# Optimization experiments

Measured on AMD Instinct MI355X. Metric: run time of the kernel, lower is better.

## Reference

```python
import jax, jax.numpy as jnp
import numpy as np

B = 4096          # batch
N_REPS = 16       # number of irreducible reps (all same d here)
N_ELEMS = 128     # group elements per rep
D = 32            # block dimension
N_SYMBOLS = 64    # alphabet size
EMB = N_REPS * D * D  # 16384


def setup_inputs() -> dict:
    key = jax.random.key(0)
    k1, k2, k3, k4 = jax.random.split(key, 4)
    state_embedding = jax.random.normal(k1, (B, EMB), dtype=jnp.float32)
    input_symbols = jax.random.randint(k2, (B,), 0, N_SYMBOLS, dtype=jnp.int64)
    reps = jax.random.normal(k3, (N_REPS, N_ELEMS, D, D), dtype=jnp.float32)
    transitions = jax.random.randint(k4, (N_SYMBOLS,), 0, N_ELEMS, dtype=jnp.int64)
    return {"state_embedding": state_embedding, "input_symbols": input_symbols,
            "reps": reps, "transitions": transitions}


def reference(state_embedding, input_symbols, reps, transitions):
    # state_embedding: [B, n_reps*d*d]; reps: [n_reps, n_elems, d, d]
    n_reps, n_elems, d, _ = reps.shape
    b = state_embedding.shape[0]
    # Split embedding into block-diagonal d x d blocks (all reps same d).
    blocks = jnp.nan_to_num(state_embedding.reshape(b, n_reps, d, d))  # [b, r, d, d]
    # Per-symbol gather: symbol -> group element -> rep matrix.
    t = transitions[input_symbols]            # [b]
    M = jnp.nan_to_num(reps[:, t])            # [r, b, d, d]
    # Per-matrix Frobenius normalization (matches rep_matrix.norm()).
    fro = jnp.sqrt(jnp.sum(M * M, axis=(-2, -1), keepdims=True))
    M = M / (fro + 1e-6)
    # Block-diagonal batched matmul: block @ rep_matrix per (batch, rep).
    out = jnp.einsum('brij,rbjk->brik', blocks, M)  # [b, r, d, d]
    return out.reshape(b, -1)
```

## Files before the change

kernel.cpp:

```cpp
#include <hip/hip_runtime.h>
#include <hip/hip_bf16.h>

#define NREPS   16
#define NELEMS  128
#define DD      32
#define MATSZ   (DD * DD)
#define EMB     (NREPS * MATSZ)

typedef __attribute__((ext_vector_type(8))) short bf16x8;
typedef __attribute__((ext_vector_type(4))) float f32x4;

static __device__ __forceinline__ short f2bf(float f) {
    __hip_bfloat16 h = __float2bfloat16(f);
    return *reinterpret_cast<short*>(&h);
}

__global__ __launch_bounds__(256) void prep_kernel(
    const float* __restrict__ reps, ushort* __restrict__ Mt)
{
    __shared__ float lM[DD * 33];
    __shared__ float red[4];
    const int mat = blockIdx.x;
    const int t   = threadIdx.x;

    float4 v = reinterpret_cast<const float4*>(reps + (size_t)mat * MATSZ)[t];
    const int i  = t >> 3;
    const int c0 = (t & 7) << 2;
    lM[i * 33 + c0 + 0] = v.x;
    lM[i * 33 + c0 + 1] = v.y;
    lM[i * 33 + c0 + 2] = v.z;
    lM[i * 33 + c0 + 3] = v.w;

    float s = v.x * v.x + v.y * v.y + v.z * v.z + v.w * v.w;
    #pragma unroll
    for (int off = 32; off; off >>= 1) s += __shfl_xor(s, off, 64);
    if ((t & 63) == 0) red[t >> 6] = s;
    __syncthreads();
    const float scale = 1.0f / (sqrtf(red[0] + red[1] + red[2] + red[3]) + 1e-6f);

    const int col = t >> 3;
    const int k0  = (t & 7) << 2;
    ushort4 o;
    o.x = (ushort)f2bf(lM[(k0 + 0) * 33 + col] * scale);
    o.y = (ushort)f2bf(lM[(k0 + 1) * 33 + col] * scale);
    o.z = (ushort)f2bf(lM[(k0 + 2) * 33 + col] * scale);
    o.w = (ushort)f2bf(lM[(k0 + 3) * 33 + col] * scale);
    reinterpret_cast<ushort4*>(Mt + (size_t)mat * MATSZ)[t] = o;
}

__global__ __launch_bounds__(256, 4) void trans_mfma4_kernel(
    const float*  __restrict__ emb,
    const int*    __restrict__ syms,
    const ushort* __restrict__ Mt,
    const int*    __restrict__ trans,
    float*        __restrict__ out)
{
    const int b = blockIdx.x;
    const int w = threadIdx.x >> 6;
    const int l = threadIdx.x & 63;
    const int rr = w << 2;

    const int esym = trans[syms[b]];
    const int lr = l & 15;
    const int k0 = (l >> 4) << 3;

    const float*  A0 = emb + (size_t)b * EMB + (size_t)rr * MATSZ;
    const ushort* M0 = Mt + ((size_t)rr * NELEMS + esym) * MATSZ;

    float4 alo[4][2], ahi[4][2];
    bf16x8 bfg[4][2];
    #pragma unroll
    for (int p = 0; p < 4; ++p) {
        const float*  A = A0 + p * MATSZ;
        const ushort* M = M0 + (size_t)p * NELEMS * MATSZ;
        #pragma unroll
        for (int ti = 0; ti < 2; ++ti) {
            const float* ap = A + (ti * 16 + lr) * DD + k0;
            alo[p][ti] = *reinterpret_cast<const float4*>(ap);
            ahi[p][ti] = *reinterpret_cast<const float4*>(ap + 4);
        }
        #pragma unroll
        for (int tj = 0; tj < 2; ++tj)
            bfg[p][tj] = *reinterpret_cast<const bf16x8*>(M + (tj * 16 + lr) * DD + k0);
    }

    const f32x4 z = {0.0f, 0.0f, 0.0f, 0.0f};
    const int row0 = (l >> 4) << 2;

    #pragma unroll
    for (int p = 0; p < 4; ++p) {
        bf16x8 af[2];
        #pragma unroll
        for (int ti = 0; ti < 2; ++ti) {
            bf16x8 f;
            f[0] = f2bf(alo[p][ti].x); f[1] = f2bf(alo[p][ti].y);
            f[2] = f2bf(alo[p][ti].z); f[3] = f2bf(alo[p][ti].w);
            f[4] = f2bf(ahi[p][ti].x); f[5] = f2bf(ahi[p][ti].y);
            f[6] = f2bf(ahi[p][ti].z); f[7] = f2bf(ahi[p][ti].w);
            af[ti] = f;
        }

        f32x4 acc[2][2];
        #pragma unroll
        for (int ti = 0; ti < 2; ++ti)
            #pragma unroll
            for (int tj = 0; tj < 2; ++tj)
                acc[ti][tj] = __builtin_amdgcn_mfma_f32_16x16x32_bf16(
                    af[ti], bfg[p][tj], z, 0, 0, 0);

        float* Ob = out + (size_t)b * EMB + (size_t)(rr + p) * MATSZ;
        #pragma unroll
        for (int ti = 0; ti < 2; ++ti)
            #pragma unroll
            for (int m = 0; m < 4; ++m) {
                const int row = ti * 16 + row0 + m;
                #pragma unroll
                for (int tj = 0; tj < 2; ++tj)
                    __builtin_nontemporal_store(acc[ti][tj][m],
                                                Ob + row * DD + tj * 16 + lr);
            }
    }
}

extern "C" void kernel_launch(void* const* d_in, const int* in_sizes, int n_in,
                              void* d_out, int out_size, void* d_ws, size_t ws_size,
                              hipStream_t stream) {
    const float* emb   = (const float*)d_in[0];
    const int*   syms  = (const int*)d_in[1];
    const float* reps  = (const float*)d_in[2];
    const int*   trans = (const int*)d_in[3];
    float*  outp = (float*)d_out;
    ushort* Mt   = (ushort*)d_ws;

    const int B = in_sizes[1];

    hipLaunchKernelGGL(prep_kernel, dim3(NREPS * NELEMS), dim3(256), 0, stream,
                       reps, Mt);
    hipLaunchKernelGGL(trans_mfma4_kernel, dim3(B), dim3(256), 0, stream,
                       emb, syms, Mt, trans, outp);
}
```

Baseline: 119.9 us.

## Double-buffer per-matrix loads and process two batch rows per block

Replaces the load-everything-then-compute scheme with a two-slot register double buffer. Loads for the next matrix are issued while the current one is converted, multiplied and stored. Each block now covers two batch rows (8 matrices per wave), which halves the grid and lowers peak register use. The launch-bounds occupancy hint is dropped, so there are fewer loads in flight per wave, and the gain depends on the compiler keeping the loads ahead of the stores.

```diff
diff --git a/kernel.cpp b/kernel.cpp
--- a/kernel.cpp
+++ b/kernel.cpp
@@ -48,77 +48,99 @@
     reinterpret_cast<ushort4*>(Mt + (size_t)mat * MATSZ)[t] = o;
 }
 
-__global__ __launch_bounds__(256, 4) void trans_mfma4_kernel(
+struct RegSet {
+    float4 alo[2], ahi[2];
+    bf16x8 mt[2];
+};
+
+static __device__ __forceinline__ void issue_loads(
+    RegSet& s, const float* __restrict__ A, const ushort* __restrict__ M,
+    int lr, int k0)
+{
+    #pragma unroll
+    for (int ti = 0; ti < 2; ++ti) {
+        const float* ap = A + (ti * 16 + lr) * DD + k0;
+        s.alo[ti] = *reinterpret_cast<const float4*>(ap);
+        s.ahi[ti] = *reinterpret_cast<const float4*>(ap + 4);
+    }
+    #pragma unroll
+    for (int tj = 0; tj < 2; ++tj)
+        s.mt[tj] = *reinterpret_cast<const bf16x8*>(M + (tj * 16 + lr) * DD + k0);
+}
+
+static __device__ __forceinline__ void compute_store(
+    const RegSet& s, float* __restrict__ Ob, int lr, int row0)
+{
+    bf16x8 af[2];
+    #pragma unroll
+    for (int ti = 0; ti < 2; ++ti) {
+        bf16x8 f;
+        f[0] = f2bf(s.alo[ti].x); f[1] = f2bf(s.alo[ti].y);
+        f[2] = f2bf(s.alo[ti].z); f[3] = f2bf(s.alo[ti].w);
+        f[4] = f2bf(s.ahi[ti].x); f[5] = f2bf(s.ahi[ti].y);
+        f[6] = f2bf(s.ahi[ti].z); f[7] = f2bf(s.ahi[ti].w);
+        af[ti] = f;
+    }
+    const f32x4 z = {0.0f, 0.0f, 0.0f, 0.0f};
+    f32x4 acc[2][2];
+    #pragma unroll
+    for (int ti = 0; ti < 2; ++ti)
+        #pragma unroll
+        for (int tj = 0; tj < 2; ++tj)
+            acc[ti][tj] = __builtin_amdgcn_mfma_f32_16x16x32_bf16(
+                af[ti], s.mt[tj], z, 0, 0, 0);
+    #pragma unroll
+    for (int ti = 0; ti < 2; ++ti)
+        #pragma unroll
+        for (int m = 0; m < 4; ++m) {
+            const int row = ti * 16 + row0 + m;
+            #pragma unroll
+            for (int tj = 0; tj < 2; ++tj)
+                __builtin_nontemporal_store(acc[ti][tj][m],
+                                            Ob + row * DD + tj * 16 + lr);
+        }
+}
+
+__global__ __launch_bounds__(256) void trans_mfma_pipe_kernel(
     const float*  __restrict__ emb,
     const int*    __restrict__ syms,
     const ushort* __restrict__ Mt,
     const int*    __restrict__ trans,
     float*        __restrict__ out)
 {
-    const int b = blockIdx.x;
-    const int w = threadIdx.x >> 6;
-    const int l = threadIdx.x & 63;
-    const int rr = w << 2;
-
-    const int esym = trans[syms[b]];
-    const int lr = l & 15;
-    const int k0 = (l >> 4) << 3;
-
-    const float*  A0 = emb + (size_t)b * EMB + (size_t)rr * MATSZ;
-    const ushort* M0 = Mt + ((size_t)rr * NELEMS + esym) * MATSZ;
-
-    float4 alo[4][2], ahi[4][2];
-    bf16x8 bfg[4][2];
-    #pragma unroll
-    for (int p = 0; p < 4; ++p) {
-        const float*  A = A0 + p * MATSZ;
-        const ushort* M = M0 + (size_t)p * NELEMS * MATSZ;
-        #pragma unroll
-        for (int ti = 0; ti < 2; ++ti) {
-            const float* ap = A + (ti * 16 + lr) * DD + k0;
-            alo[p][ti] = *reinterpret_cast<const float4*>(ap);
-            ahi[p][ti] = *reinterpret_cast<const float4*>(ap + 4);
-        }
-        #pragma unroll
-        for (int tj = 0; tj < 2; ++tj)
-            bfg[p][tj] = *reinterpret_cast<const bf16x8*>(M + (tj * 16 + lr) * DD + k0);
-    }
-
-    const f32x4 z = {0.0f, 0.0f, 0.0f, 0.0f};
+    const int b0 = blockIdx.x << 1;
+    const int w  = threadIdx.x >> 6;
+    const int l  = threadIdx.x & 63;
+    const int lr   = l & 15;
+    const int k0   = (l >> 4) << 3;
     const int row0 = (l >> 4) << 2;
 
+    const int e0 = trans[syms[b0]];
+    const int e1 = trans[syms[b0 + 1]];
+
+    auto Aptr = [&](int i) {
+        return emb + (size_t)(b0 + (i >> 2)) * EMB
+                   + (size_t)((w << 2) + (i & 3)) * MATSZ;
+    };
+    auto Mptr = [&](int i) {
+        return Mt + ((size_t)((w << 2) + (i & 3)) * NELEMS
+                     + ((i >> 2) ? e1 : e0)) * MATSZ;
+    };
+    auto Optr = [&](int i) {
+        return out + (size_t)(b0 + (i >> 2)) * EMB
+                   + (size_t)((w << 2) + (i & 3)) * MATSZ;
+    };
+
+    RegSet s0, s1;
+    issue_loads(s0, Aptr(0), Mptr(0), lr, k0);
+
     #pragma unroll
-    for (int p = 0; p < 4; ++p) {
-        bf16x8 af[2];
-        #pragma unroll
-        for (int ti = 0; ti < 2; ++ti) {
-            bf16x8 f;
-            f[0] = f2bf(alo[p][ti].x); f[1] = f2bf(alo[p][ti].y);
-            f[2] = f2bf(alo[p][ti].z); f[3] = f2bf(alo[p][ti].w);
-            f[4] = f2bf(ahi[p][ti].x); f[5] = f2bf(ahi[p][ti].y);
-            f[6] = f2bf(ahi[p][ti].z); f[7] = f2bf(ahi[p][ti].w);
-            af[ti] = f;
-        }
-
-        f32x4 acc[2][2];
-        #pragma unroll
-        for (int ti = 0; ti < 2; ++ti)
-            #pragma unroll
-            for (int tj = 0; tj < 2; ++tj)
-                acc[ti][tj] = __builtin_amdgcn_mfma_f32_16x16x32_bf16(
-                    af[ti], bfg[p][tj], z, 0, 0, 0);
-
-        float* Ob = out + (size_t)b * EMB + (size_t)(rr + p) * MATSZ;
-        #pragma unroll
-        for (int ti = 0; ti < 2; ++ti)
-            #pragma unroll
-            for (int m = 0; m < 4; ++m) {
-                const int row = ti * 16 + row0 + m;
-                #pragma unroll
-                for (int tj = 0; tj < 2; ++tj)
-                    __builtin_nontemporal_store(acc[ti][tj][m],
-                                                Ob + row * DD + tj * 16 + lr);
-            }
+    for (int it = 0; it < 8; it += 2) {
+        issue_loads(s1, Aptr(it + 1), Mptr(it + 1), lr, k0);
+        compute_store(s0, Optr(it), lr, row0);
+        if (it + 2 < 8)
+            issue_loads(s0, Aptr(it + 2), Mptr(it + 2), lr, k0);
+        compute_store(s1, Optr(it + 1), lr, row0);
     }
 }
 
@@ -136,6 +158,6 @@
 
     hipLaunchKernelGGL(prep_kernel, dim3(NREPS * NELEMS), dim3(256), 0, stream,
                        reps, Mt);
-    hipLaunchKernelGGL(trans_mfma4_kernel, dim3(B), dim3(256), 0, stream,
+    hipLaunchKernelGGL(trans_mfma_pipe_kernel, dim3(B / 2), dim3(256), 0, stream,
                        emb, syms, Mt, trans, outp);
 }
```

New measurement: 120.9 us. No clear change (+0.8%).

## Stage embedding blocks via async global-to-LDS DMA with double buffering

Applied to the files above, without the earlier changes.

The main kernel now loads each rep's fp32 embedding block with global_load_lds into an XOR-swizzled shared-memory double buffer. It prefetches the next block and the next bf16 rep matrix while the current one is converted and multiplied. Before, all four blocks per wave were held in registers up front. The aim is to cut register pressure and overlap loads with MFMA and stores. It adds 32KB of LDS per block and depends on hand-written vmcnt waits, which could be fragile if the compiler reorders memory ops or if the nontemporal stores are counted in vmcnt.

```diff
diff --git a/kernel.cpp b/kernel.cpp
--- a/kernel.cpp
+++ b/kernel.cpp
@@ -10,9 +10,16 @@
 typedef __attribute__((ext_vector_type(8))) short bf16x8;
 typedef __attribute__((ext_vector_type(4))) float f32x4;
 
+typedef __attribute__((address_space(3))) void lds_void;
+typedef __attribute__((address_space(1))) void glb_void;
+
 static __device__ __forceinline__ short f2bf(float f) {
     __hip_bfloat16 h = __float2bfloat16(f);
     return *reinterpret_cast<short*>(&h);
+}
+
+static __device__ __forceinline__ void gload16(const void* g, void* l) {
+    __builtin_amdgcn_global_load_lds((glb_void*)g, (lds_void*)l, 16, 0, 0);
 }
 
 __global__ __launch_bounds__(256) void prep_kernel(
@@ -48,55 +55,76 @@
     reinterpret_cast<ushort4*>(Mt + (size_t)mat * MATSZ)[t] = o;
 }
 
-__global__ __launch_bounds__(256, 4) void trans_mfma4_kernel(
+__global__ __launch_bounds__(256) void trans_dma_kernel(
     const float*  __restrict__ emb,
     const int*    __restrict__ syms,
     const ushort* __restrict__ Mt,
     const int*    __restrict__ trans,
     float*        __restrict__ out)
 {
+    __shared__ float lA[8 * MATSZ];
     const int b = blockIdx.x;
     const int w = threadIdx.x >> 6;
     const int l = threadIdx.x & 63;
-    const int rr = w << 2;
 
+    const int lr   = l & 15;
+    const int k0   = (l >> 4) << 3;
+    const int row0 = (l >> 4) << 2;
     const int esym = trans[syms[b]];
-    const int lr = l & 15;
-    const int k0 = (l >> 4) << 3;
 
-    const float*  A0 = emb + (size_t)b * EMB + (size_t)rr * MATSZ;
-    const ushort* M0 = Mt + ((size_t)rr * NELEMS + esym) * MATSZ;
+    const float* Ab    = emb + (size_t)b * EMB + (size_t)(w << 2) * MATSZ;
+    float*       lslot = lA + w * 2 * MATSZ;
 
-    float4 alo[4][2], ahi[4][2];
-    bf16x8 bfg[4][2];
-    #pragma unroll
-    for (int p = 0; p < 4; ++p) {
-        const float*  A = A0 + p * MATSZ;
-        const ushort* M = M0 + (size_t)p * NELEMS * MATSZ;
+    auto stage = [&](int p, int s) {
+        const float* Am = Ab + (size_t)p * MATSZ;
+        float* ldsb = lslot + s * MATSZ;
         #pragma unroll
-        for (int ti = 0; ti < 2; ++ti) {
-            const float* ap = A + (ti * 16 + lr) * DD + k0;
-            alo[p][ti] = *reinterpret_cast<const float4*>(ap);
-            ahi[p][ti] = *reinterpret_cast<const float4*>(ap + 4);
+        for (int j = 0; j < 4; ++j) {
+            const int tp  = j * 64 + l;
+            const int row = tp >> 3;
+            const int c   = tp & 7;
+            const int gc  = (row << 3) | (c ^ (row & 7));
+            gload16(Am + gc * 4, ldsb + j * 256);
         }
+    };
+    auto loadMt = [&](int p, bf16x8* dst) {
+        const ushort* M = Mt + ((size_t)((w << 2) + p) * NELEMS + esym) * MATSZ;
         #pragma unroll
         for (int tj = 0; tj < 2; ++tj)
-            bfg[p][tj] = *reinterpret_cast<const bf16x8*>(M + (tj * 16 + lr) * DD + k0);
-    }
+            dst[tj] = *reinterpret_cast<const bf16x8*>(M + (tj * 16 + lr) * DD + k0);
+    };
+
+    bf16x8 mtA[2], mtB[2];
+    stage(0, 0);
+    loadMt(0, mtA);
 
     const f32x4 z = {0.0f, 0.0f, 0.0f, 0.0f};
-    const int row0 = (l >> 4) << 2;
+    const int s7  = lr & 7;
+    const int clo = (l >> 4) << 1;
 
     #pragma unroll
     for (int p = 0; p < 4; ++p) {
+        if (p < 3) {
+            stage(p + 1, (p + 1) & 1);
+            if (p & 1) loadMt(p + 1, mtA); else loadMt(p + 1, mtB);
+        }
+        if (p < 3) asm volatile("s_waitcnt vmcnt(6)" ::: "memory");
+        else       asm volatile("s_waitcnt vmcnt(0)" ::: "memory");
+
+        const float* ldsm = lslot + (p & 1) * MATSZ;
         bf16x8 af[2];
         #pragma unroll
         for (int ti = 0; ti < 2; ++ti) {
+            const int row = ti * 16 + lr;
+            f32x4 lo = *reinterpret_cast<const f32x4*>(
+                ldsm + ((row << 3) | (clo ^ s7)) * 4);
+            f32x4 hi = *reinterpret_cast<const f32x4*>(
+                ldsm + ((row << 3) | ((clo + 1) ^ s7)) * 4);
             bf16x8 f;
-            f[0] = f2bf(alo[p][ti].x); f[1] = f2bf(alo[p][ti].y);
-            f[2] = f2bf(alo[p][ti].z); f[3] = f2bf(alo[p][ti].w);
-            f[4] = f2bf(ahi[p][ti].x); f[5] = f2bf(ahi[p][ti].y);
-            f[6] = f2bf(ahi[p][ti].z); f[7] = f2bf(ahi[p][ti].w);
+            f[0] = f2bf(lo[0]); f[1] = f2bf(lo[1]);
+            f[2] = f2bf(lo[2]); f[3] = f2bf(lo[3]);
+            f[4] = f2bf(hi[0]); f[5] = f2bf(hi[1]);
+            f[6] = f2bf(hi[2]); f[7] = f2bf(hi[3]);
             af[ti] = f;
         }
 
@@ -106,9 +134,9 @@
             #pragma unroll
             for (int tj = 0; tj < 2; ++tj)
                 acc[ti][tj] = __builtin_amdgcn_mfma_f32_16x16x32_bf16(
-                    af[ti], bfg[p][tj], z, 0, 0, 0);
+                    af[ti], (p & 1) ? mtB[tj] : mtA[tj], z, 0, 0, 0);
 
-        float* Ob = out + (size_t)b * EMB + (size_t)(rr + p) * MATSZ;
+        float* Ob = out + (size_t)b * EMB + (size_t)((w << 2) + p) * MATSZ;
         #pragma unroll
         for (int ti = 0; ti < 2; ++ti)
             #pragma unroll
@@ -136,6 +164,6 @@
 
     hipLaunchKernelGGL(prep_kernel, dim3(NREPS * NELEMS), dim3(256), 0, stream,
                        reps, Mt);
-    hipLaunchKernelGGL(trans_mfma4_kernel, dim3(B), dim3(256), 0, stream,
+    hipLaunchKernelGGL(trans_dma_kernel, dim3(B), dim3(256), 0, stream,
                        emb, syms, Mt, trans, outp);
 }
```

New measurement: 111.1 us. -7.3%, faster.
